# Optimization experiments

Measured on AMD Instinct MI355X. Metric: run time of the kernel, lower is better.

## Reference

```python
import jax, jax.numpy as jnp
import numpy as np

B, S, H, UNITS = 32, 2048, 1024, 1024

def setup_inputs() -> dict:
    key = jax.random.key(0)
    ks = jax.random.split(key, 8)
    sc_h = 1.0 / np.sqrt(H)
    sc_u = 1.0 / np.sqrt(UNITS)
    return {
        "query": jax.random.normal(ks[0], (B, H), jnp.float32),
        "values": jax.random.normal(ks[1], (B, S, H), jnp.float32),
        "W1": jax.random.normal(ks[2], (H, UNITS), jnp.float32) * sc_h,
        "b1": jnp.zeros((UNITS,), jnp.float32),
        "W2": jax.random.normal(ks[3], (H, UNITS), jnp.float32) * sc_h,
        "b2": jnp.zeros((UNITS,), jnp.float32),
        "V": jax.random.normal(ks[4], (UNITS, 1), jnp.float32) * sc_u,
        "bv": jnp.zeros((1,), jnp.float32),
    }

def reference(query, values, W1, b1, W2, b2, V, bv):
    # W1(values): [B,S,U]; W2(query)[:,None,:]: [B,1,U] broadcast-added
    proj = jnp.tanh(
        jnp.einsum("bsh,hu->bsu", values, W1) + b1
        + (query @ W2 + b2)[:, None, :]
    )
    score = proj @ V + bv                      # [B,S,1]
    attention_weights = jax.nn.softmax(score, axis=1)  # softmax over seq
    context_vector = jnp.sum(attention_weights * values, axis=1)  # [B,H]
    return context_vector, attention_weights
```

## Files before the change

kernel.cpp:

```cpp
#include <hip/hip_runtime.h>
#include <hip/hip_bf16.h>


#define B_ 32
#define S_ 2048
#define H_ 1024
#define U_ 1024
#define M_ (B_ * S_)
#define NT_ 32

typedef __bf16 bf16;
typedef __bf16 bf16x8 __attribute__((ext_vector_type(8)));
typedef float  f32x4  __attribute__((ext_vector_type(4)));

__device__ __forceinline__ void gl2lds16(const void* g, void* l) {
    __builtin_amdgcn_global_load_lds(
        (const __attribute__((address_space(1))) void*)g,
        (__attribute__((address_space(3))) void*)l, 16, 0, 0);
}

__device__ __forceinline__ bf16x8 cvt8(float4 a, float4 b) {
    bf16x8 o;
    o[0] = (bf16)a.x; o[1] = (bf16)a.y; o[2] = (bf16)a.z; o[3] = (bf16)a.w;
    o[4] = (bf16)b.x; o[5] = (bf16)b.y; o[6] = (bf16)b.z; o[7] = (bf16)b.w;
    return o;
}

__global__ void prep_kernel(const float* __restrict__ W1, bf16* __restrict__ W1T,
                            const float* __restrict__ query, const float* __restrict__ W2,
                            const float* __restrict__ b2, float* __restrict__ q2,
                            const float* __restrict__ values, bf16* __restrict__ vbf) {
    __shared__ __align__(16) char smem[64 * 65 * 2];
    int tid = threadIdx.x;
    if (blockIdx.x < 256) {
        bf16* t = (bf16*)smem;
        int h0 = (blockIdx.x >> 4) * 64, u0 = (blockIdx.x & 15) * 64;
        #pragma unroll
        for (int i = 0; i < 16; ++i) {
            int idx = i * 256 + tid;
            int r = idx >> 6, c = idx & 63;
            t[c * 65 + r] = (bf16)W1[(long)(h0 + r) * U_ + u0 + c];
        }
        __syncthreads();
        #pragma unroll
        for (int i = 0; i < 16; ++i) {
            int idx = i * 256 + tid;
            int r = idx >> 6, c = idx & 63;
            W1T[(long)(u0 + r) * H_ + h0 + c] = t[r * 65 + c];
        }
    } else if (blockIdx.x < 768) {
        float* qsh  = (float*)smem;
        float* part = (float*)(smem + 4096);
        int idx = blockIdx.x - 256;
        int b  = idx >> 4;
        int u0 = (idx & 15) * 64;
        int ul = tid & 63, kc = tid >> 6;
        for (int i = tid; i < H_; i += 256) qsh[i] = query[b * H_ + i];
        __syncthreads();
        float acc = 0.f;
        const float* wp = W2 + (long)(kc * 256) * U_ + u0 + ul;
        #pragma unroll 8
        for (int h = 0; h < 256; ++h) acc += qsh[kc * 256 + h] * wp[(long)h * U_];
        part[kc * 64 + ul] = acc;
        __syncthreads();
        if (tid < 64)
            q2[b * U_ + u0 + tid] = part[tid] + part[64 + tid] + part[128 + tid]
                                    + part[192 + tid] + b2[u0 + tid];
    } else {
        long cid = (long)(blockIdx.x - 768) * 256 + tid;
        const long stride = 4096L * 256;
        const long n8 = (long)M_ * H_ / 8;
        for (long c = cid; c < n8; c += stride) {
            const float4* s = reinterpret_cast<const float4*>(values + c * 8);
            float4 a = s[0], b = s[1];
            *reinterpret_cast<bf16x8*>(vbf + c * 8) = cvt8(a, b);
        }
    }
}

__global__ __launch_bounds__(512, 2) void score_gemm8(
    const bf16* __restrict__ A,
    const bf16* __restrict__ BT,
    const float* __restrict__ b1, const float* __restrict__ q2,
    const float* __restrict__ V, float* __restrict__ score )
{
    __shared__ __align__(16) bf16 lds[65536];
    const int tid  = threadIdx.x;
    const int lane = tid & 63;
    const int wave = tid >> 6;
    const int wm = wave >> 2, wn = wave & 3;
    const int lrow = lane & 15, quad = lane >> 4;

    const int xcd = blockIdx.x & 7;
    const int j   = blockIdx.x >> 3;
    const int mt  = xcd * 32 + (j >> 2);
    const int nt  = j & 3;
    const long m0 = (long)mt * 256;
    const int  n0 = nt * 256;

    const int rs = wave * 16 + (lane >> 2);
    const int sl = (lane & 3) ^ ((lane >> 3) & 3);
    const bf16* ag0 = A  + (m0 + rs) * H_ + sl * 8;
    const bf16* ag1 = ag0 + 128 * H_;
    const bf16* bg0 = BT + (long)(n0 + rs) * H_ + sl * 8;
    const bf16* bg1 = bg0 + 128 * H_;

    const int kse  = (quad ^ ((lrow >> 1) & 3)) * 8;
    const int aoff = (wm * 128 + lrow) * 32 + kse;
    const int boff = 8192 + (wn * 64 + lrow) * 32 + kse;

    f32x4 acc[8][4];
    const f32x4 zero = {0.f, 0.f, 0.f, 0.f};
    #pragma unroll
    for (int mi = 0; mi < 8; ++mi)
        #pragma unroll
        for (int ni = 0; ni < 4; ++ni) acc[mi][ni] = zero;

    for (int tt = 0; tt < 3; ++tt) {
        bf16* d = lds + tt * 16384 + wave * 512;
        gl2lds16(ag0 + tt * 32, d);
        gl2lds16(ag1 + tt * 32, d + 4096);
        gl2lds16(bg0 + tt * 32, d + 8192);
        gl2lds16(bg1 + tt * 32, d + 8192 + 4096);
    }
    __builtin_amdgcn_sched_barrier(0);
    asm volatile("s_waitcnt vmcnt(8)" ::: "memory");
    __builtin_amdgcn_s_barrier();
    __builtin_amdgcn_sched_barrier(0);

    bf16x8 bgA[4], a0A[4], bgB[4], a0B[4], af1[4];

    #pragma unroll
    for (int ni = 0; ni < 4; ++ni)
        bgA[ni] = *reinterpret_cast<const bf16x8*>(lds + boff + ni * 512);
    #pragma unroll
    for (int mi = 0; mi < 4; ++mi)
        a0A[mi] = *reinterpret_cast<const bf16x8*>(lds + aoff + mi * 512);

#define TILE_BODY(T, bgC, a0C, bgN, a0N) do {                                   \
    const int t_ = (T);                                                         \
    const bf16* buf_ = lds + (t_ & 3) * 16384;                                  \
     \
    if (t_ + 3 < NT_) {                                                         \
        bf16* d_ = lds + ((t_ + 3) & 3) * 16384 + wave * 512;                   \
        gl2lds16(ag0 + (t_ + 3) * 32, d_);                                      \
        gl2lds16(ag1 + (t_ + 3) * 32, d_ + 4096);                               \
    }                                                                           \
    _Pragma("unroll")                                                           \
    for (int mi = 0; mi < 4; ++mi)                                              \
        af1[mi] = *reinterpret_cast<const bf16x8*>(buf_ + aoff + (4+mi) * 512); \
    asm volatile("s_waitcnt lgkmcnt(4)" ::: "memory");                          \
    __builtin_amdgcn_sched_barrier(0);                                          \
    __builtin_amdgcn_s_setprio(1);                                              \
    _Pragma("unroll")                                                           \
    for (int mi = 0; mi < 4; ++mi)                                              \
        _Pragma("unroll")                                                       \
        for (int ni = 0; ni < 4; ++ni)                                          \
            acc[mi][ni] = __builtin_amdgcn_mfma_f32_16x16x32_bf16(              \
                a0C[mi], bgC[ni], acc[mi][ni], 0, 0, 0);                        \
    __builtin_amdgcn_s_setprio(0);                                              \
    __builtin_amdgcn_sched_barrier(0);                                          \
             \
    if (t_ < NT_ - 3)       asm volatile("s_waitcnt vmcnt(6)" ::: "memory");    \
    else if (t_ == NT_ - 3) asm volatile("s_waitcnt vmcnt(4)" ::: "memory");    \
    else if (t_ == NT_ - 2) asm volatile("s_waitcnt vmcnt(0)" ::: "memory");    \
    __builtin_amdgcn_s_barrier();                                               \
    __builtin_amdgcn_sched_barrier(0);                                          \
            \
    if (t_ + 3 < NT_) {                                                         \
        bf16* d_ = lds + ((t_ + 3) & 3) * 16384 + 8192 + wave * 512;            \
        gl2lds16(bg0 + (t_ + 3) * 32, d_);                                      \
        gl2lds16(bg1 + (t_ + 3) * 32, d_ + 4096);                               \
    }                                                                           \
    if (t_ + 1 < NT_) {                                                         \
        const bf16* nb_ = lds + ((t_ + 1) & 3) * 16384;                         \
        _Pragma("unroll")                                                       \
        for (int ni = 0; ni < 4; ++ni)                                          \
            bgN[ni] = *reinterpret_cast<const bf16x8*>(nb_ + boff + ni * 512);  \
        _Pragma("unroll")                                                       \
        for (int mi = 0; mi < 4; ++mi)                                          \
            a0N[mi] = *reinterpret_cast<const bf16x8*>(nb_ + aoff + mi * 512);  \
        asm volatile("s_waitcnt lgkmcnt(8)" ::: "memory");                      \
    } else {                                                                    \
        asm volatile("s_waitcnt lgkmcnt(0)" ::: "memory");                      \
    }                                                                           \
    __builtin_amdgcn_sched_barrier(0);                                          \
    __builtin_amdgcn_s_setprio(1);                                              \
    _Pragma("unroll")                                                           \
    for (int mi = 0; mi < 4; ++mi)                                              \
        _Pragma("unroll")                                                       \
        for (int ni = 0; ni < 4; ++ni)                                          \
            acc[4+mi][ni] = __builtin_amdgcn_mfma_f32_16x16x32_bf16(            \
                af1[mi], bgC[ni], acc[4+mi][ni], 0, 0, 0);                      \
    __builtin_amdgcn_s_setprio(0);                                              \
    __builtin_amdgcn_sched_barrier(0);                                          \
} while (0)

    #pragma unroll 1
    for (int tp = 0; tp < NT_; tp += 2) {
        TILE_BODY(tp,     bgA, a0A, bgB, a0B);
        TILE_BODY(tp + 1, bgB, a0B, bgA, a0A);
    }
#undef TILE_BODY

    const int bb = (int)(m0 / S_);
    float bq[4], vv[4];
    #pragma unroll
    for (int ni = 0; ni < 4; ++ni) {
        int u = n0 + wn * 64 + ni * 16 + lrow;
        bq[ni] = b1[u] + q2[bb * U_ + u];
        vv[ni] = V[u];
    }
    #pragma unroll
    for (int mi = 0; mi < 8; ++mi) {
        #pragma unroll
        for (int r = 0; r < 4; ++r) {
            float s = 0.f;
            #pragma unroll
            for (int ni = 0; ni < 4; ++ni) {
                float x = acc[mi][ni][r] + bq[ni];
                float th = 1.f - 2.f / (__expf(2.f * x) + 1.f);
                s += th * vv[ni];
            }
            s += __shfl_xor(s, 1); s += __shfl_xor(s, 2);
            s += __shfl_xor(s, 4); s += __shfl_xor(s, 8);
            if (lrow == 0)
                atomicAdd(score + m0 + wm * 128 + mi * 16 + quad * 4 + r, s);
        }
    }
}

#define ASTRIDE 40
__global__ __launch_bounds__(256, 3) void score_gemm(
    const float* __restrict__ A32,
    const bf16* __restrict__ BT,
    const float* __restrict__ b1, const float* __restrict__ q2,
    const float* __restrict__ V, float* __restrict__ score )
{
    __shared__ __align__(16) bf16 a_sh[2 * 128 * ASTRIDE];
    __shared__ __align__(16) bf16 b_sh[2 * 128 * 32];
    const int tid  = threadIdx.x;
    const int lane = tid & 63;
    const int wave = tid >> 6;
    const int wm = wave >> 1, wn = wave & 1;
    const int xcd = blockIdx.x & 7;
    const int i_  = blockIdx.x >> 3;
    const int nt  = i_ & 7;
    const int mt  = xcd * 64 + (i_ >> 3);
    const long m0 = (long)mt * 128;
    const int  n0 = nt * 128;
    const int lrow = lane & 15;
    const int quad = lane >> 4;
    const int arow = tid >> 1;
    const int aseg = tid & 1;

    f32x4 acc[4][4];
    const f32x4 zero = {0.f, 0.f, 0.f, 0.f};
    #pragma unroll
    for (int mi = 0; mi < 4; ++mi)
        #pragma unroll
        for (int ni = 0; ni < 4; ++ni) acc[mi][ni] = zero;

    const float* Abase = A32 + m0 * H_;
    const bf16*  Bbase = BT + (long)n0 * H_;

    for (int kt = 0; kt < H_; kt += 64) {
        #pragma unroll
        for (int i = 0; i < 4; ++i) {
            int g  = i * 4 + wave;
            int hs = g >> 3, q = g & 7;
            int row = q * 16 + (lane >> 2);
            int gc  = (lane & 3) ^ ((row >> 1) & 3);
            gl2lds16(Bbase + (long)row * H_ + kt + hs * 32 + gc * 8,
                     (void*)(b_sh + hs * 4096 + q * 512));
        }
        float4 av[2][4];
        #pragma unroll
        for (int hs = 0; hs < 2; ++hs) {
            const float4* src = reinterpret_cast<const float4*>(
                Abase + (long)arow * H_ + kt + hs * 32 + aseg * 16);
            av[hs][0] = src[0]; av[hs][1] = src[1];
            av[hs][2] = src[2]; av[hs][3] = src[3];
        }
        #pragma unroll
        for (int hs = 0; hs < 2; ++hs) {
            bf16* dst = a_sh + hs * (128 * ASTRIDE) + arow * ASTRIDE + aseg * 16;
            *reinterpret_cast<bf16x8*>(dst)     = cvt8(av[hs][0], av[hs][1]);
            *reinterpret_cast<bf16x8*>(dst + 8) = cvt8(av[hs][2], av[hs][3]);
        }
        __syncthreads();

        #pragma unroll
        for (int hs = 0; hs < 2; ++hs) {
            bf16x8 af[4], bg[4];
            #pragma unroll
            for (int mi = 0; mi < 4; ++mi) {
                int r = wm * 64 + mi * 16 + lrow;
                af[mi] = *reinterpret_cast<const bf16x8*>(
                    a_sh + hs * (128 * ASTRIDE) + r * ASTRIDE + quad * 8);
            }
            #pragma unroll
            for (int ni = 0; ni < 4; ++ni) {
                int r = wn * 64 + ni * 16 + lrow;
                int p = quad ^ ((r >> 1) & 3);
                bg[ni] = *reinterpret_cast<const bf16x8*>(
                    b_sh + hs * 4096 + r * 32 + p * 8);
            }
            #pragma unroll
            for (int mi = 0; mi < 4; ++mi)
                #pragma unroll
                for (int ni = 0; ni < 4; ++ni)
                    acc[mi][ni] = __builtin_amdgcn_mfma_f32_16x16x32_bf16(
                        af[mi], bg[ni], acc[mi][ni], 0, 0, 0);
        }
        __syncthreads();
    }

    const int bb = (int)(m0 / S_);
    float bq[4], vv[4];
    #pragma unroll
    for (int ni = 0; ni < 4; ++ni) {
        int u = n0 + wn * 64 + ni * 16 + lrow;
        bq[ni] = b1[u] + q2[bb * U_ + u];
        vv[ni] = V[u];
    }
    #pragma unroll
    for (int mi = 0; mi < 4; ++mi) {
        #pragma unroll
        for (int r = 0; r < 4; ++r) {
            float s = 0.f;
            #pragma unroll
            for (int ni = 0; ni < 4; ++ni) {
                float x = acc[mi][ni][r] + bq[ni];
                float t = 1.f - 2.f / (__expf(2.f * x) + 1.f);
                s += t * vv[ni];
            }
            s += __shfl_xor(s, 1); s += __shfl_xor(s, 2);
            s += __shfl_xor(s, 4); s += __shfl_xor(s, 8);
            if (lrow == 0)
                atomicAdd(score + m0 + wm * 64 + mi * 16 + quad * 4 + r, s);
        }
    }
}

__global__ void softmax_kernel(float* __restrict__ attn) {
    __shared__ float sh[S_];
    __shared__ float red[8];
    int b = blockIdx.x, tid = threadIdx.x;
    float* row = attn + (long)b * S_;
    float lmax = -1e30f;
    for (int i = tid; i < S_; i += 256) { float v = row[i]; sh[i] = v; lmax = fmaxf(lmax, v); }
    #pragma unroll
    for (int m = 32; m; m >>= 1) lmax = fmaxf(lmax, __shfl_xor(lmax, m));
    if ((tid & 63) == 0) red[tid >> 6] = lmax;
    __syncthreads();
    float gmax = fmaxf(fmaxf(red[0], red[1]), fmaxf(red[2], red[3]));
    float lsum = 0.f;
    for (int i = tid; i < S_; i += 256) { float e = __expf(sh[i] - gmax); sh[i] = e; lsum += e; }
    #pragma unroll
    for (int m = 32; m; m >>= 1) lsum += __shfl_xor(lsum, m);
    if ((tid & 63) == 0) red[4 + (tid >> 6)] = lsum;
    __syncthreads();
    float inv = 1.f / (red[4] + red[5] + red[6] + red[7]);
    for (int i = tid; i < S_; i += 256) row[i] = sh[i] * inv;
}

__global__ void context_kernel(const float* __restrict__ vals, const float* __restrict__ attn,
                               float* __restrict__ ctx ) {
    __shared__ float a_sh[128];
    int b = blockIdx.x >> 4;
    int sc = blockIdx.x & 15;
    int tid = threadIdx.x;
    if (tid < 128) a_sh[tid] = attn[(long)b * S_ + sc * 128 + tid];
    __syncthreads();
    const float* base = vals + ((long)b * S_ + sc * 128) * H_ + tid * 4;
    float ax = 0.f, ay = 0.f, az = 0.f, aw = 0.f;
    #pragma unroll 4
    for (int s = 0; s < 128; ++s) {
        float w = a_sh[s];
        float4 v = *reinterpret_cast<const float4*>(base + (long)s * H_);
        ax += w * v.x; ay += w * v.y; az += w * v.z; aw += w * v.w;
    }
    float* c = ctx + (long)b * H_ + tid * 4;
    atomicAdd(c + 0, ax); atomicAdd(c + 1, ay);
    atomicAdd(c + 2, az); atomicAdd(c + 3, aw);
}

extern "C" void kernel_launch(void* const* d_in, const int* in_sizes, int n_in,
                              void* d_out, int out_size, void* d_ws, size_t ws_size,
                              hipStream_t stream) {
    const float* query  = (const float*)d_in[0];
    const float* values = (const float*)d_in[1];
    const float* W1     = (const float*)d_in[2];
    const float* b1     = (const float*)d_in[3];
    const float* W2     = (const float*)d_in[4];
    const float* b2     = (const float*)d_in[5];
    const float* V      = (const float*)d_in[6];

    char* ws = (char*)d_ws;
    bf16*  w1t = (bf16*)ws;
    float* q2  = (float*)(ws + (size_t)U_ * H_ * 2);
    bf16*  vbf = (bf16*)(ws + (size_t)U_ * H_ * 2 + (size_t)B_ * U_ * 4);
    const size_t need = (size_t)U_ * H_ * 2 + (size_t)B_ * U_ * 4
                      + (size_t)M_ * H_ * 2;

    float* ctx  = (float*)d_out;
    float* attn = (float*)d_out + B_ * H_;

    hipMemsetAsync(d_out, 0, (size_t)(B_ * H_ + B_ * S_) * sizeof(float), stream);

    if (ws_size >= need) {
        prep_kernel <<<768 + 4096, 256, 0, stream>>>(W1, w1t, query, W2, b2, q2, values, vbf);
        score_gemm8 <<<1024,       512, 0, stream>>>(vbf, w1t, b1, q2, V, attn);
    } else {
        prep_kernel <<<768,        256, 0, stream>>>(W1, w1t, query, W2, b2, q2, values, vbf);
        score_gemm  <<<(M_ / 128) * 8, 256, 0, stream>>>(values, w1t, b1, q2, V, attn);
    }
    softmax_kernel<<<B_,      256, 0, stream>>>(attn);
    context_kernel<<<B_ * 16, 256, 0, stream>>>(values, attn, ctx);
}
```

Before: 592.1 us.

## Switch score GEMM to 32x32x16 MFMA, fuse output zeroing, split context wider

Replaces the 16x16x32 bf16 MFMA tiling in the score GEMM with 32x32x16 MFMAs, which changes the LDS fragment addressing and the epilogue reduction that turns tanh·V into a score per row. The output memset moves into extra blocks of the prep kernel, removing a separate launch. The context kernel now splits the sequence into 64 chunks instead of 16, giving more blocks and more memory parallelism at the cost of more atomics. The larger MFMA shape is meant to raise matrix throughput per issued instruction, but it brings a different register footprint and wider shuffle reductions.

```diff
diff --git a/kernel.cpp b/kernel.cpp
--- a/kernel.cpp
+++ b/kernel.cpp
@@ -12,6 +12,7 @@
 typedef __bf16 bf16;
 typedef __bf16 bf16x8 __attribute__((ext_vector_type(8)));
 typedef float  f32x4  __attribute__((ext_vector_type(4)));
+typedef float  f32x16 __attribute__((ext_vector_type(16)));
 
 __device__ __forceinline__ void gl2lds16(const void* g, void* l) {
     __builtin_amdgcn_global_load_lds(
@@ -29,7 +30,8 @@
 __global__ void prep_kernel(const float* __restrict__ W1, bf16* __restrict__ W1T,
                             const float* __restrict__ query, const float* __restrict__ W2,
                             const float* __restrict__ b2, float* __restrict__ q2,
-                            const float* __restrict__ values, bf16* __restrict__ vbf) {
+                            const float* __restrict__ values, bf16* __restrict__ vbf,
+                            float* __restrict__ dout) {
     __shared__ __align__(16) char smem[64 * 65 * 2];
     int tid = threadIdx.x;
     if (blockIdx.x < 256) {
@@ -66,7 +68,7 @@
         if (tid < 64)
             q2[b * U_ + u0 + tid] = part[tid] + part[64 + tid] + part[128 + tid]
                                     + part[192 + tid] + b2[u0 + tid];
-    } else {
+    } else if (blockIdx.x < 4864) {
         long cid = (long)(blockIdx.x - 768) * 256 + tid;
         const long stride = 4096L * 256;
         const long n8 = (long)M_ * H_ / 8;
@@ -75,6 +77,10 @@
             float4 a = s[0], b = s[1];
             *reinterpret_cast<bf16x8*>(vbf + c * 8) = cvt8(a, b);
         }
+    } else {
+        int cid = (blockIdx.x - 4864) * 256 + tid;
+        float4 z = {0.f, 0.f, 0.f, 0.f};
+        reinterpret_cast<float4*>(dout)[cid] = z;
     }
 }
 
@@ -89,7 +95,7 @@
     const int lane = tid & 63;
     const int wave = tid >> 6;
     const int wm = wave >> 2, wn = wave & 3;
-    const int lrow = lane & 15, quad = lane >> 4;
+    const int l31 = lane & 31, hi5 = lane >> 5;
 
     const int xcd = blockIdx.x & 7;
     const int j   = blockIdx.x >> 3;
@@ -105,16 +111,20 @@
     const bf16* bg0 = BT + (long)(n0 + rs) * H_ + sl * 8;
     const bf16* bg1 = bg0 + 128 * H_;
 
-    const int kse  = (quad ^ ((lrow >> 1) & 3)) * 8;
-    const int aoff = (wm * 128 + lrow) * 32 + kse;
-    const int boff = 8192 + (wn * 64 + lrow) * 32 + kse;
-
-    f32x4 acc[8][4];
-    const f32x4 zero = {0.f, 0.f, 0.f, 0.f};
-    #pragma unroll
-    for (int mi = 0; mi < 8; ++mi)
-        #pragma unroll
-        for (int ni = 0; ni < 4; ++ni) acc[mi][ni] = zero;
+    const int key = (l31 >> 1) & 3;
+    const int s0  = (hi5 ^ key) * 8;
+    const int s1  = ((2 | hi5) ^ key) * 8;
+    const int aoff = (wm * 128 + l31) * 32;
+    const int boff = 8192 + (wn * 64 + l31) * 32;
+
+    f32x16 acc[4][2];
+    {
+        f32x16 z{};
+        #pragma unroll
+        for (int mi = 0; mi < 4; ++mi)
+            #pragma unroll
+            for (int ni = 0; ni < 2; ++ni) acc[mi][ni] = z;
+    }
 
     for (int tt = 0; tt < 3; ++tt) {
         bf16* d = lds + tt * 16384 + wave * 512;
@@ -131,11 +141,15 @@
     bf16x8 bgA[4], a0A[4], bgB[4], a0B[4], af1[4];
 
     #pragma unroll
-    for (int ni = 0; ni < 4; ++ni)
-        bgA[ni] = *reinterpret_cast<const bf16x8*>(lds + boff + ni * 512);
-    #pragma unroll
-    for (int mi = 0; mi < 4; ++mi)
-        a0A[mi] = *reinterpret_cast<const bf16x8*>(lds + aoff + mi * 512);
+    for (int jj = 0; jj < 4; ++jj)
+        bgA[jj] = *reinterpret_cast<const bf16x8*>(
+            lds + boff + (jj >> 1) * 1024 + ((jj & 1) ? s1 : s0));
+    #pragma unroll
+    for (int jj = 0; jj < 4; ++jj)
+        a0A[jj] = *reinterpret_cast<const bf16x8*>(
+            lds + aoff + (jj >> 1) * 1024 + ((jj & 1) ? s1 : s0));
+
+#define MFMA32(a, b, c) __builtin_amdgcn_mfma_f32_32x32x16_bf16(a, b, c, 0, 0, 0)
 
 #define TILE_BODY(T, bgC, a0C, bgN, a0N) do {                                   \
     const int t_ = (T);                                                         \
@@ -147,17 +161,19 @@
         gl2lds16(ag1 + (t_ + 3) * 32, d_ + 4096);                               \
     }                                                                           \
     _Pragma("unroll")                                                           \
-    for (int mi = 0; mi < 4; ++mi)                                              \
-        af1[mi] = *reinterpret_cast<const bf16x8*>(buf_ + aoff + (4+mi) * 512); \
+    for (int jj = 0; jj < 4; ++jj)                                              \
+        af1[jj] = *reinterpret_cast<const bf16x8*>(                             \
+            buf_ + aoff + (2 + (jj >> 1)) * 1024 + ((jj & 1) ? s1 : s0));       \
     asm volatile("s_waitcnt lgkmcnt(4)" ::: "memory");                          \
     __builtin_amdgcn_sched_barrier(0);                                          \
     __builtin_amdgcn_s_setprio(1);                                              \
     _Pragma("unroll")                                                           \
-    for (int mi = 0; mi < 4; ++mi)                                              \
+    for (int mi = 0; mi < 2; ++mi)                                              \
         _Pragma("unroll")                                                       \
-        for (int ni = 0; ni < 4; ++ni)                                          \
-            acc[mi][ni] = __builtin_amdgcn_mfma_f32_16x16x32_bf16(              \
-                a0C[mi], bgC[ni], acc[mi][ni], 0, 0, 0);                        \
+        for (int ni = 0; ni < 2; ++ni) {                                        \
+            acc[mi][ni] = MFMA32(a0C[mi*2+0], bgC[ni*2+0], acc[mi][ni]);        \
+            acc[mi][ni] = MFMA32(a0C[mi*2+1], bgC[ni*2+1], acc[mi][ni]);        \
+        }                                                                       \
     __builtin_amdgcn_s_setprio(0);                                              \
     __builtin_amdgcn_sched_barrier(0);                                          \
              \
@@ -166,7 +182,7 @@
     else if (t_ == NT_ - 2) asm volatile("s_waitcnt vmcnt(0)" ::: "memory");    \
     __builtin_amdgcn_s_barrier();                                               \
     __builtin_amdgcn_sched_barrier(0);                                          \
-            \
+             \
     if (t_ + 3 < NT_) {                                                         \
         bf16* d_ = lds + ((t_ + 3) & 3) * 16384 + 8192 + wave * 512;            \
         gl2lds16(bg0 + (t_ + 3) * 32, d_);                                      \
@@ -175,11 +191,13 @@
     if (t_ + 1 < NT_) {                                                         \
         const bf16* nb_ = lds + ((t_ + 1) & 3) * 16384;                         \
         _Pragma("unroll")                                                       \
-        for (int ni = 0; ni < 4; ++ni)                                          \
-            bgN[ni] = *reinterpret_cast<const bf16x8*>(nb_ + boff + ni * 512);  \
+        for (int jj = 0; jj < 4; ++jj)                                          \
+            bgN[jj] = *reinterpret_cast<const bf16x8*>(                         \
+                nb_ + boff + (jj >> 1) * 1024 + ((jj & 1) ? s1 : s0));          \
         _Pragma("unroll")                                                       \
-        for (int mi = 0; mi < 4; ++mi)                                          \
-            a0N[mi] = *reinterpret_cast<const bf16x8*>(nb_ + aoff + mi * 512);  \
+        for (int jj = 0; jj < 4; ++jj)                                          \
+            a0N[jj] = *reinterpret_cast<const bf16x8*>(                         \
+                nb_ + aoff + (jj >> 1) * 1024 + ((jj & 1) ? s1 : s0));          \
         asm volatile("s_waitcnt lgkmcnt(8)" ::: "memory");                      \
     } else {                                                                    \
         asm volatile("s_waitcnt lgkmcnt(0)" ::: "memory");                      \
@@ -187,11 +205,12 @@
     __builtin_amdgcn_sched_barrier(0);                                          \
     __builtin_amdgcn_s_setprio(1);                                              \
     _Pragma("unroll")                                                           \
-    for (int mi = 0; mi < 4; ++mi)                                              \
+    for (int mi = 0; mi < 2; ++mi)                                              \
         _Pragma("unroll")                                                       \
-        for (int ni = 0; ni < 4; ++ni)                                          \
-            acc[4+mi][ni] = __builtin_amdgcn_mfma_f32_16x16x32_bf16(            \
-                af1[mi], bgC[ni], acc[4+mi][ni], 0, 0, 0);                      \
+        for (int ni = 0; ni < 2; ++ni) {                                        \
+            acc[2+mi][ni] = MFMA32(af1[mi*2+0], bgC[ni*2+0], acc[2+mi][ni]);    \
+            acc[2+mi][ni] = MFMA32(af1[mi*2+1], bgC[ni*2+1], acc[2+mi][ni]);    \
+        }                                                                       \
     __builtin_amdgcn_s_setprio(0);                                              \
     __builtin_amdgcn_sched_barrier(0);                                          \
 } while (0)
@@ -202,30 +221,31 @@
         TILE_BODY(tp + 1, bgB, a0B, bgA, a0A);
     }
 #undef TILE_BODY
+#undef MFMA32
 
     const int bb = (int)(m0 / S_);
-    float bq[4], vv[4];
-    #pragma unroll
-    for (int ni = 0; ni < 4; ++ni) {
-        int u = n0 + wn * 64 + ni * 16 + lrow;
+    float bq[2], vv[2];
+    #pragma unroll
+    for (int ni = 0; ni < 2; ++ni) {
+        int u = n0 + wn * 64 + ni * 32 + l31;
         bq[ni] = b1[u] + q2[bb * U_ + u];
         vv[ni] = V[u];
     }
     #pragma unroll
-    for (int mi = 0; mi < 8; ++mi) {
-        #pragma unroll
-        for (int r = 0; r < 4; ++r) {
-            float s = 0.f;
-            #pragma unroll
-            for (int ni = 0; ni < 4; ++ni) {
-                float x = acc[mi][ni][r] + bq[ni];
-                float th = 1.f - 2.f / (__expf(2.f * x) + 1.f);
-                s += th * vv[ni];
+    for (int mi = 0; mi < 4; ++mi) {
+        #pragma unroll
+        for (int reg = 0; reg < 16; ++reg) {
+            float x0 = acc[mi][0][reg] + bq[0];
+            float x1 = acc[mi][1][reg] + bq[1];
+            float s = (1.f - 2.f / (__expf(2.f * x0) + 1.f)) * vv[0]
+                    + (1.f - 2.f / (__expf(2.f * x1) + 1.f)) * vv[1];
+            s += __shfl_xor(s, 1);  s += __shfl_xor(s, 2);
+            s += __shfl_xor(s, 4);  s += __shfl_xor(s, 8);
+            s += __shfl_xor(s, 16);
+            if (l31 == 0) {
+                int row = (reg & 3) + 8 * (reg >> 2) + 4 * hi5;
+                atomicAdd(score + m0 + wm * 128 + mi * 32 + row, s);
             }
-            s += __shfl_xor(s, 1); s += __shfl_xor(s, 2);
-            s += __shfl_xor(s, 4); s += __shfl_xor(s, 8);
-            if (lrow == 0)
-                atomicAdd(score + m0 + wm * 128 + mi * 16 + quad * 4 + r, s);
         }
     }
 }
@@ -367,16 +387,16 @@
 
 __global__ void context_kernel(const float* __restrict__ vals, const float* __restrict__ attn,
                                float* __restrict__ ctx ) {
-    __shared__ float a_sh[128];
-    int b = blockIdx.x >> 4;
-    int sc = blockIdx.x & 15;
+    __shared__ float a_sh[32];
+    int b  = blockIdx.x >> 6;
+    int sc = blockIdx.x & 63;
     int tid = threadIdx.x;
-    if (tid < 128) a_sh[tid] = attn[(long)b * S_ + sc * 128 + tid];
+    if (tid < 32) a_sh[tid] = attn[(long)b * S_ + sc * 32 + tid];
     __syncthreads();
-    const float* base = vals + ((long)b * S_ + sc * 128) * H_ + tid * 4;
+    const float* base = vals + ((long)b * S_ + sc * 32) * H_ + tid * 4;
     float ax = 0.f, ay = 0.f, az = 0.f, aw = 0.f;
     #pragma unroll 4
-    for (int s = 0; s < 128; ++s) {
+    for (int s = 0; s < 32; ++s) {
         float w = a_sh[s];
         float4 v = *reinterpret_cast<const float4*>(base + (long)s * H_);
         ax += w * v.x; ay += w * v.y; az += w * v.z; aw += w * v.w;
@@ -407,15 +427,16 @@
     float* ctx  = (float*)d_out;
     float* attn = (float*)d_out + B_ * H_;
 
-    hipMemsetAsync(d_out, 0, (size_t)(B_ * H_ + B_ * S_) * sizeof(float), stream);
-
     if (ws_size >= need) {
-        prep_kernel <<<768 + 4096, 256, 0, stream>>>(W1, w1t, query, W2, b2, q2, values, vbf);
-        score_gemm8 <<<1024,       512, 0, stream>>>(vbf, w1t, b1, q2, V, attn);
+        prep_kernel <<<4960, 256, 0, stream>>>(W1, w1t, query, W2, b2, q2, values, vbf,
+                                               (float*)d_out);
+        score_gemm8 <<<1024, 512, 0, stream>>>(vbf, w1t, b1, q2, V, attn);
     } else {
-        prep_kernel <<<768,        256, 0, stream>>>(W1, w1t, query, W2, b2, q2, values, vbf);
+        hipMemsetAsync(d_out, 0, (size_t)(B_ * H_ + B_ * S_) * sizeof(float), stream);
+        prep_kernel <<<768, 256, 0, stream>>>(W1, w1t, query, W2, b2, q2, values, vbf,
+                                              (float*)d_out);
         score_gemm  <<<(M_ / 128) * 8, 256, 0, stream>>>(values, w1t, b1, q2, V, attn);
     }
     softmax_kernel<<<B_,      256, 0, stream>>>(attn);
-    context_kernel<<<B_ * 16, 256, 0, stream>>>(values, attn, ctx);
-}
+    context_kernel<<<B_ * 64, 256, 0, stream>>>(values, attn, ctx);
+}
```

Measured after the change: 642.9 us. +8.6%, slower.
